# Optimization experiments

Measured on AMD Instinct MI355X. Metric: run time of the kernel, lower is better.

## Reference

```python
import jax, jax.numpy as jnp
import numpy as np

T, N, E = 8, 50000, 800000
XD, HD, GD, ZD, TD, YHD = 128, 256, 128, 128, 8, 16
PSH = 100          # ps_predictor hidden width
BN_EPS = 1e-5


def _dense(k, fan_in, shape):
    return jax.random.normal(k, shape, jnp.float32) * (1.0 / np.sqrt(fan_in))


def setup_inputs() -> dict:
    ks = jax.random.split(jax.random.key(0), 20)
    inp = {}
    inp["X"] = jax.random.normal(ks[0], (T, N, XD), jnp.float32)
    inp["C"] = jax.random.uniform(ks[1], (T, N, TD), dtype=jnp.float32)
    inp["Y_hist"] = jax.random.normal(ks[2], (T, N, YHD), jnp.float32)
    inp["edge_index"] = jax.random.randint(ks[3], (T, 2, E), 0, N)
    # parameters
    inp["phi_W"] = _dense(ks[4], XD, (XD, HD)); inp["phi_b"] = jnp.zeros((HD,), jnp.float32)
    inp["gc_W"] = _dense(ks[5], HD, (T, HD, GD)); inp["gc_b"] = jnp.zeros((T, GD), jnp.float32)
    inp["ew_logit"] = jax.random.normal(ks[6], (T, E), jnp.float32) * 0.1  # learned edge weights (pre-sigmoid)
    inp["fuse_W"] = _dense(ks[7], 2 * HD + GD, (2 * HD + GD, ZD)); inp["fuse_b"] = jnp.zeros((ZD,), jnp.float32)
    inp["o00_W"] = _dense(ks[8], ZD, (ZD, ZD)); inp["o00_b"] = jnp.zeros((ZD,), jnp.float32)
    inp["o10_W"] = _dense(ks[9], ZD, (ZD, ZD)); inp["o10_b"] = jnp.zeros((ZD,), jnp.float32)
    inp["o01_W"] = _dense(ks[10], ZD, (ZD, 1)); inp["o01_b"] = jnp.zeros((1,), jnp.float32)
    inp["o11_W"] = _dense(ks[11], ZD, (ZD, 1)); inp["o11_b"] = jnp.zeros((1,), jnp.float32)
    inp["ps1_W"] = _dense(ks[12], ZD, (ZD, PSH)); inp["ps1_b"] = jnp.zeros((PSH,), jnp.float32)
    inp["bn_g"] = jnp.ones((PSH,), jnp.float32); inp["bn_b"] = jnp.zeros((PSH,), jnp.float32)
    inp["ps2_W"] = _dense(ks[13], PSH, (PSH, 2)); inp["ps2_b"] = jnp.zeros((2,), jnp.float32)
    inp["gru_Wih"] = _dense(ks[14], ZD + TD + YHD, (3 * HD, ZD + TD + YHD))
    inp["gru_Whh"] = _dense(ks[15], HD, (3 * HD, HD))
    inp["gru_bih"] = jnp.zeros((3 * HD,), jnp.float32)
    inp["gru_bhh"] = jnp.zeros((3 * HD,), jnp.float32)
    return inp


def reference(X, C, Y_hist, edge_index, phi_W, phi_b, gc_W, gc_b, ew_logit,
              fuse_W, fuse_b, o00_W, o00_b, o10_W, o10_b, o01_W, o01_b,
              o11_W, o11_b, ps1_W, ps1_b, bn_g, bn_b, ps2_W, ps2_b,
              gru_Wih, gru_Whh, gru_bih, gru_bhh):
    h0 = jnp.zeros((N, HD), X.dtype)
    bn_scale = bn_g / jnp.sqrt(1.0 + BN_EPS)  # eval-mode BN: running_mean=0, running_var=1

    def step(h, xs):
        x, ei, c, yh, W_t, b_t, ewl_t = xs
        phi = jax.nn.relu(x @ phi_W + phi_b)                              # [N,HD]
        # --- GCNConv with learned sigmoid edge weights + self loops ---
        src, dst = ei[0], ei[1]
        ew = jax.nn.sigmoid(ewl_t)                                        # [E]
        deg = jax.ops.segment_sum(ew, dst, num_segments=N) + 1.0          # +1 for self-loop weight
        dinv = jax.lax.rsqrt(deg)
        norm = dinv[src] * ew * dinv[dst]                                 # symmetric norm per edge
        xw = phi @ W_t                                                    # [N,GD]
        agg = jax.ops.segment_sum(norm[:, None] * xw[src], dst, num_segments=N)
        agg = agg + xw / deg[:, None] + b_t                               # self-loop contribution + bias
        rep = jax.nn.relu(agg)                                            # [N,GD] (dropout off in eval)
        # --- fuse with skip connection ---
        z = jax.nn.relu(jnp.concatenate([h, rep, phi], axis=1) @ fuse_W + fuse_b)  # [N,ZD]
        # --- GRUCell (torch gate order: reset, update, new) ---
        inp = jnp.concatenate([z, c, yh], axis=1)
        gi = inp @ gru_Wih.T + gru_bih
        gh = h @ gru_Whh.T + gru_bhh
        i_r, i_z, i_n = jnp.split(gi, 3, axis=1)
        h_r, h_z, h_n = jnp.split(gh, 3, axis=1)
        r = jax.nn.sigmoid(i_r + h_r)
        u = jax.nn.sigmoid(i_z + h_z)
        n = jnp.tanh(i_n + r * h_n)
        h_new = (1.0 - u) * n + u * h
        # --- outcome heads ---
        y0 = jax.nn.relu(z @ o00_W + o00_b) @ o01_W + o01_b               # [N,1]
        y1 = jax.nn.relu(z @ o10_W + o10_b) @ o11_W + o11_b               # [N,1]
        # --- propensity head (BatchNorm eval, sigmoid, softmax) ---
        s = jax.nn.sigmoid((z @ ps1_W + ps1_b) * bn_scale + bn_b)
        ps = jax.nn.softmax(s @ ps2_W + ps2_b, axis=1)                    # [N,2]
        return h_new, (y1, y0, z, ps)

    h_fin, (all_y1, all_y0, all_z, all_ps) = jax.lax.scan(
        step, h0, (X, edge_index, C, Y_hist, gc_W, gc_b, ew_logit))
    return all_y1, all_y0, all_z, all_ps, h_fin
```

## Files before the change

### kernel.cpp

```cpp
#include <hip/hip_runtime.h>
#include <math.h>

#define T_STEPS 8
#define NN 50000
#define EE 800000
#define TN (T_STEPS*NN)
#define TE (T_STEPS*EE)

typedef unsigned int uint;
typedef unsigned short ushort;
typedef unsigned long long u64;
typedef __attribute__((ext_vector_type(8))) short short8;
typedef __attribute__((ext_vector_type(4))) float f32x4;

__device__ __forceinline__ float sigf(float x){ return 1.0f/(1.0f+expf(-x)); }
__device__ __forceinline__ ushort f2b(float f){
  uint x = __float_as_uint(f);
  uint r = (x + 0x7fffu + ((x>>16)&1u)) >> 16;
  return (ushort)r;
}
__device__ __forceinline__ float b2f(ushort u){ return __uint_as_float(((uint)u)<<16); }

__device__ __forceinline__ void gload16(const ushort* g, ushort* l){
  __builtin_amdgcn_global_load_lds(
      (const __attribute__((address_space(1))) void*)g,
      (__attribute__((address_space(3))) void*)l, 16, 0, 0);
}

template<int ROWS>
__device__ __forceinline__ void stage_tile(const ushort* base, int ld, int rowclamp,
                                           ushort* lds, int lane, int wid){
  constexpr int ITERS = ROWS/32;
#pragma unroll
  for (int i=0;i<ITERS;i++){
    int lin = i*256 + wid*64 + lane;
    int row = lin>>3, s = lin&7;
    int gr = row; if (gr > rowclamp) gr = rowclamp;
    const ushort* gp = base + (size_t)gr*ld + ((s ^ (row&7))<<3);
    gload16(gp, lds + (size_t)(i*256 + wid*64)*8);
  }
}

template<int ROWS>
__device__ __forceinline__ void stage512(const ushort* base, int ld, int rowclamp,
                                         ushort* lds, int tid){
  constexpr int ITERS = ROWS/64;
#pragma unroll
  for (int i=0;i<ITERS;i++){
    int lin = i*512 + tid;
    int row = lin>>3, s = lin&7;
    int gr = row; if (gr > rowclamp) gr = rowclamp;
    const ushort* gp = base + (size_t)gr*ld + ((s ^ (row&7))<<3);
    gload16(gp, lds + (size_t)lin*8);
  }
}

__device__ __forceinline__ short8 fragld(const ushort* lds, int R, int kk, int lane){
  int slot = (kk*4 + (lane>>4)) ^ (R&7);
  return *(const short8*)&lds[R*64 + slot*8];
}

struct Seg { const ushort* p; int ld; long ts; int w; };

__global__ __launch_bounds__(256,2) void gemm_bf(
    Seg s0, Seg s1, Seg s2,
    const ushort* __restrict__ W, int K2, long Wts,
    const float* __restrict__ bias, int act,
    const ushort* __restrict__ addp, int ldad, long adts,
    float* __restrict__ C32, int ldc, long c32ts,
    ushort* __restrict__ C16, int ldb, long c16ts,
    int Nrow, int NOvalid)
{
  __shared__ __align__(16) ushort As[8192];
  __shared__ __align__(16) ushort Bs[8192];
  const int t    = blockIdx.z;
  const int tid  = threadIdx.x;
  const int lane = tid & 63;
  const int wid  = __builtin_amdgcn_readfirstlane(tid >> 6);
  const int brow = blockIdx.x*128;
  const int bcol = blockIdx.y*128;
  const int wr = wid>>1, wc = wid&1;

  f32x4 acc[4][4];
#pragma unroll
  for(int m=0;m<4;m++)
#pragma unroll
    for(int n=0;n<4;n++) acc[m][n] = (f32x4){0.f,0.f,0.f,0.f};

  const int nk = K2 >> 6;
  for (int kt=0; kt<nk; ++kt){
    int col0 = kt*64;
    const ushort* ab; int ald;
    if (col0 < s0.w){ ab = s0.p + (size_t)t*s0.ts + col0; ald = s0.ld; }
    else if (col0 < s0.w + s1.w){ ab = s1.p + (size_t)t*s1.ts + (col0 - s0.w); ald = s1.ld; }
    else { ab = s2.p + (size_t)t*s2.ts + (col0 - s0.w - s1.w); ald = s2.ld; }
    stage_tile<128>(ab + (size_t)brow*ald, ald, Nrow-1-brow, As, lane, wid);
    stage_tile<128>(W + (size_t)t*Wts + (size_t)bcol*K2 + col0, K2, 1<<30, Bs, lane, wid);
    __syncthreads();
#pragma unroll
    for (int kk=0;kk<2;kk++){
      short8 a[4], b[4];
#pragma unroll
      for (int m=0;m<4;m++) a[m] = fragld(As, wr*64 + m*16 + (lane&15), kk, lane);
#pragma unroll
      for (int n=0;n<4;n++) b[n] = fragld(Bs, wc*64 + n*16 + (lane&15), kk, lane);
#pragma unroll
      for (int m=0;m<4;m++)
#pragma unroll
        for (int n=0;n<4;n++)
          acc[m][n] = __builtin_amdgcn_mfma_f32_16x16x32_bf16(a[m], b[n], acc[m][n], 0,0,0);
    }
    __syncthreads();
  }
  const int rbase = brow + wr*64 + (lane>>4)*4;
  const int cbase = bcol + wc*64 + (lane&15);
#pragma unroll
  for (int m=0;m<4;m++){
#pragma unroll
    for (int q=0;q<4;q++){
      int r = rbase + m*16 + q;
      if (r >= Nrow) continue;
#pragma unroll
      for (int n=0;n<4;n++){
        int c = cbase + n*16;
        if (c >= NOvalid) continue;
        float v = acc[m][n][q];
        if (addp) v += b2f(addp[(size_t)t*adts + (size_t)r*ldad + c]);
        if (bias) v += bias[c];
        if (act==1) v = fmaxf(v, 0.f);
        if (C32) C32[(size_t)t*c32ts + (size_t)r*ldc + c] = v;
        if (C16) C16[(size_t)t*c16ts + (size_t)r*ldb + c] = f2b(v);
      }
    }
  }
}

__global__ __launch_bounds__(512,2) void gemm_phi512(
    const float* __restrict__ A32,
    const ushort* __restrict__ W,
    const float* __restrict__ bias,
    ushort* __restrict__ C16, long c16ts,
    int Nrow)
{
  __shared__ __align__(16) ushort As[8192];
  __shared__ __align__(16) ushort Bs[16384];
  const int t    = blockIdx.z;
  const int tid  = threadIdx.x;
  const int lane = tid & 63;
  const int wid  = __builtin_amdgcn_readfirstlane(tid >> 6);
  const int brow = blockIdx.x*128;
  const int wr = wid>>2, wc = wid&3;
  const float* At = A32 + (size_t)t*NN*128;

  f32x4 acc[4][4];
#pragma unroll
  for(int m=0;m<4;m++)
#pragma unroll
    for(int n=0;n<4;n++) acc[m][n] = (f32x4){0.f,0.f,0.f,0.f};

  for (int kt=0; kt<2; ++kt){
    int col0 = kt*64;
#pragma unroll
    for (int it=0; it<4; ++it){
      int lin = it*512 + tid;
      int row = lin>>4, q4 = lin&15;
      int grow = brow + row; if (grow >= Nrow) grow = Nrow-1;
      float4 v = *(const float4*)&At[(size_t)grow*128 + col0 + q4*4];
      int s = q4>>1, half = q4&1;
      uint lo = (uint)f2b(v.x) | ((uint)f2b(v.y)<<16);
      uint hi = (uint)f2b(v.z) | ((uint)f2b(v.w)<<16);
      *(uint2*)&As[row*64 + ((s ^ (row&7))<<3) + half*4] = make_uint2(lo,hi);
    }
    stage512<256>(W + col0, 128, 1<<30, Bs, tid);
    __syncthreads();
#pragma unroll
    for (int kk=0;kk<2;kk++){
      short8 a[4], b[4];
#pragma unroll
      for (int m=0;m<4;m++) a[m] = fragld(As, wr*64 + m*16 + (lane&15), kk, lane);
#pragma unroll
      for (int n=0;n<4;n++) b[n] = fragld(Bs, wc*64 + n*16 + (lane&15), kk, lane);
#pragma unroll
      for (int m=0;m<4;m++)
#pragma unroll
        for (int n=0;n<4;n++)
          acc[m][n] = __builtin_amdgcn_mfma_f32_16x16x32_bf16(a[m], b[n], acc[m][n], 0,0,0);
    }
    __syncthreads();
  }
  const int rbase = brow + wr*64 + (lane>>4)*4;
  const int cbase = wc*64 + (lane&15);
#pragma unroll
  for (int m=0;m<4;m++){
#pragma unroll
    for (int q=0;q<4;q++){
      int r = rbase + m*16 + q;
      if (r >= Nrow) continue;
#pragma unroll
      for (int n=0;n<4;n++){
        int c = cbase + n*16;
        float v = acc[m][n][q] + bias[c];
        v = fmaxf(v, 0.f);
        C16[(size_t)t*c16ts + (size_t)r*256 + c] = f2b(v);
      }
    }
  }
}

__global__ __launch_bounds__(512,2) void gemm_gru512(
    Seg s0, Seg s1, Seg s2,
    const ushort* __restrict__ W,
    const float* __restrict__ bg,
    const float* __restrict__ hin,
    float* __restrict__ hout, ushort* __restrict__ hbfo,
    int Nrow)
{
  __shared__ __align__(16) ushort As[8192];
  __shared__ __align__(16) ushort Bs[16384];
  const int tid  = threadIdx.x;
  const int lane = tid & 63;
  const int wid  = __builtin_amdgcn_readfirstlane(tid >> 6);
  const int brow = blockIdx.x*128;
  const int bcol = blockIdx.y*256;
  const int wr = wid>>2, wc = wid&3;
  const int K2 = 448;

  f32x4 acc[4][4];
#pragma unroll
  for(int m=0;m<4;m++)
#pragma unroll
    for(int n=0;n<4;n++) acc[m][n] = (f32x4){0.f,0.f,0.f,0.f};

  for (int kt=0; kt<7; ++kt){
    int col0 = kt*64;
    const ushort* ab; int ald;
    if (col0 < s0.w){ ab = s0.p + col0; ald = s0.ld; }
    else if (col0 < s0.w + s1.w){ ab = s1.p + (col0 - s0.w); ald = s1.ld; }
    else { ab = s2.p + (col0 - s0.w - s1.w); ald = s2.ld; }
    stage512<128>(ab + (size_t)brow*ald, ald, Nrow-1-brow, As, tid);
    stage512<256>(W + (size_t)bcol*K2 + col0, K2, 1<<30, Bs, tid);
    __syncthreads();
#pragma unroll
    for (int kk=0;kk<2;kk++){
      short8 a[4], b[4];
#pragma unroll
      for (int m=0;m<4;m++) a[m] = fragld(As, wr*64 + m*16 + (lane&15), kk, lane);
#pragma unroll
      for (int n=0;n<4;n++) b[n] = fragld(Bs, wc*64 + n*16 + (lane&15), kk, lane);
#pragma unroll
      for (int m=0;m<4;m++)
#pragma unroll
        for (int n=0;n<4;n++)
          acc[m][n] = __builtin_amdgcn_mfma_f32_16x16x32_bf16(a[m], b[n], acc[m][n], 0,0,0);
    }
    __syncthreads();
  }
  const int jj = lane&15;
  const int G  = blockIdx.y*4 + wc;
  const int j  = G*16 + jj;
  const int rbase = brow + wr*64 + (lane>>4)*4;
  float bb[4];
#pragma unroll
  for (int n=0;n<4;n++) bb[n] = bg[G*64 + n*16 + jj];
#pragma unroll
  for (int m=0;m<4;m++){
#pragma unroll
    for (int q=0;q<4;q++){
      int r = rbase + m*16 + q;
      if (r >= Nrow) continue;
      float v0 = acc[m][0][q] + bb[0];
      float v1 = acc[m][1][q] + bb[1];
      float v2 = acc[m][2][q] + bb[2];
      float v3 = acc[m][3][q] + bb[3];
      float rg = sigf(v0), ug = sigf(v1);
      float ng = tanhf(v2 + rg*v3);
      float ho = hin[(size_t)r*256 + j];
      float hn = (1.f-ug)*ng + ug*ho;
      hout[(size_t)r*256 + j] = hn;
      hbfo[(size_t)r*256 + j] = f2b(hn);
    }
  }
}

__global__ __launch_bounds__(256,2) void heads_k(
    const ushort* __restrict__ Az, long Ats,
    const ushort* __restrict__ W,
    const float* __restrict__ o00b, const float* __restrict__ o10b,
    const float* __restrict__ w01, const float* __restrict__ b01,
    const float* __restrict__ w11, const float* __restrict__ b11,
    float* __restrict__ y0out, long y0ts,
    float* __restrict__ y1out, long y1ts, int Nrow)
{
  __shared__ __align__(16) ushort As[4096];
  __shared__ __align__(16) ushort Bs[16384];
  __shared__ float shy[4][64];
  const int t    = blockIdx.z;
  const int tid  = threadIdx.x;
  const int lane = tid & 63;
  const int wid  = __builtin_amdgcn_readfirstlane(tid >> 6);
  const int brow = blockIdx.x*64;
  const ushort* A = Az + (size_t)t*Ats;

  f32x4 acc[4][4];
#pragma unroll
  for(int m=0;m<4;m++)
#pragma unroll
    for(int n=0;n<4;n++) acc[m][n] = (f32x4){0.f,0.f,0.f,0.f};

  for (int kt=0; kt<2; ++kt){
    stage_tile<64>(A + (size_t)brow*128 + kt*64, 128, Nrow-1-brow, As, lane, wid);
    stage_tile<256>(W + kt*64, 128, 1<<30, Bs, lane, wid);
    __syncthreads();
#pragma unroll
    for (int kk=0;kk<2;kk++){
      short8 a[4], b[4];
#pragma unroll
      for (int m=0;m<4;m++) a[m] = fragld(As, m*16 + (lane&15), kk, lane);
#pragma unroll
      for (int n=0;n<4;n++) b[n] = fragld(Bs, wid*64 + n*16 + (lane&15), kk, lane);
#pragma unroll
      for (int m=0;m<4;m++)
#pragma unroll
        for (int n=0;n<4;n++)
          acc[m][n] = __builtin_amdgcn_mfma_f32_16x16x32_bf16(a[m], b[n], acc[m][n], 0,0,0);
    }
    __syncthreads();
  }
  float bb[4], ww[4];
#pragma unroll
  for (int n=0;n<4;n++){
    int c = wid*64 + n*16 + (lane&15);
    bb[n] = (c<128)? o00b[c] : o10b[c-128];
    ww[n] = (c<128)? w01[c]  : w11[c-128];
  }
#pragma unroll
  for (int m=0;m<4;m++){
#pragma unroll
    for (int q=0;q<4;q++){
      float p = 0.f;
#pragma unroll
      for (int n=0;n<4;n++) p += fmaxf(acc[m][n][q] + bb[n], 0.f) * ww[n];
#pragma unroll
      for (int o=1;o<16;o<<=1) p += __shfl_xor(p, o);
      if ((lane&15)==0) shy[wid][m*16 + (lane>>4)*4 + q] = p;
    }
  }
  __syncthreads();
  if (tid < 64){
    int r = brow + tid;
    if (r < Nrow){
      y0out[(size_t)t*y0ts + r] = shy[0][tid] + shy[1][tid] + b01[0];
      y1out[(size_t)t*y1ts + r] = shy[2][tid] + shy[3][tid] + b11[0];
    }
  }
}

__global__ __launch_bounds__(256,2) void ps_k(
    const ushort* __restrict__ Az, long Ats,
    const ushort* __restrict__ W,
    const float* __restrict__ psc, const float* __restrict__ psb,
    const float* __restrict__ W2, const float* __restrict__ b2,
    float* __restrict__ psout, long psts, int Nrow)
{
  __shared__ __align__(16) ushort As[8192];
  __shared__ __align__(16) ushort Bs[8192];
  __shared__ float sh0[2][128];
  __shared__ float sh1[2][128];
  const int t    = blockIdx.z;
  const int tid  = threadIdx.x;
  const int lane = tid & 63;
  const int wid  = __builtin_amdgcn_readfirstlane(tid >> 6);
  const int brow = blockIdx.x*128;
  const int wr = wid>>1, wc = wid&1;
  const ushort* A = Az + (size_t)t*Ats;

  f32x4 acc[4][4];
#pragma unroll
  for(int m=0;m<4;m++)
#pragma unroll
    for(int n=0;n<4;n++) acc[m][n] = (f32x4){0.f,0.f,0.f,0.f};

  for (int kt=0; kt<2; ++kt){
    stage_tile<128>(A + (size_t)brow*128 + kt*64, 128, Nrow-1-brow, As, lane, wid);
    stage_tile<128>(W + kt*64, 128, 1<<30, Bs, lane, wid);
    __syncthreads();
#pragma unroll
    for (int kk=0;kk<2;kk++){
      short8 a[4], b[4];
#pragma unroll
      for (int m=0;m<4;m++) a[m] = fragld(As, wr*64 + m*16 + (lane&15), kk, lane);
#pragma unroll
      for (int n=0;n<4;n++) b[n] = fragld(Bs, wc*64 + n*16 + (lane&15), kk, lane);
#pragma unroll
      for (int m=0;m<4;m++)
#pragma unroll
        for (int n=0;n<4;n++)
          acc[m][n] = __builtin_amdgcn_mfma_f32_16x16x32_bf16(a[m], b[n], acc[m][n], 0,0,0);
    }
    __syncthreads();
  }
  float sc[4], sb[4], w0_[4], w1_[4];
#pragma unroll
  for (int n=0;n<4;n++){
    int c = wc*64 + n*16 + (lane&15);
    bool ok = (c<100);
    sc[n] = ok? psc[c] : 0.f;
    sb[n] = ok? psb[c] : 0.f;
    w0_[n]= ok? W2[2*c] : 0.f;
    w1_[n]= ok? W2[2*c+1] : 0.f;
  }
#pragma unroll
  for (int m=0;m<4;m++){
#pragma unroll
    for (int q=0;q<4;q++){
      float a0=0.f, a1=0.f;
#pragma unroll
      for (int n=0;n<4;n++){
        float s = sigf(acc[m][n][q]*sc[n] + sb[n]);
        a0 += s*w0_[n]; a1 += s*w1_[n];
      }
#pragma unroll
      for (int o=1;o<16;o<<=1){ a0 += __shfl_xor(a0,o); a1 += __shfl_xor(a1,o); }
      if ((lane&15)==0){
        int rt = wr*64 + m*16 + (lane>>4)*4 + q;
        sh0[wc][rt] = a0; sh1[wc][rt] = a1;
      }
    }
  }
  __syncthreads();
  if (tid < 128){
    int r = brow + tid;
    if (r < Nrow){
      float l0 = sh0[0][tid]+sh0[1][tid]+b2[0];
      float l1 = sh1[0][tid]+sh1[1][tid]+b2[1];
      float mx = fmaxf(l0,l1);
      float e0 = expf(l0-mx), e1 = expf(l1-mx);
      float inv = 1.f/(e0+e1);
      psout[(size_t)t*psts + (size_t)r*2]   = e0*inv;
      psout[(size_t)t*psts + (size_t)r*2+1] = e1*inv;
    }
  }
}

__global__ void count_k(const int* __restrict__ ei, const float* __restrict__ ewl,
                        uint* __restrict__ degcnt, ushort* __restrict__ rank)
{
  int idx = blockIdx.x*256 + threadIdx.x;
  if (idx >= TE) return;
  int t = idx / EE;
  int e = idx - t*EE;
  const int* dst = ei + (size_t)t*2*EE + EE;
  int d = dst[e];
  uint v = (1u<<24) | (uint)(sigf(ewl[idx]) * 262144.0f);
  uint old = atomicAdd(&degcnt[t*NN + d], v);
  rank[idx] = (ushort)(old>>24);
}

__global__ void dinv_k(const uint* __restrict__ degcnt, int* __restrict__ cnt,
                       float* __restrict__ dnv, float* __restrict__ invd){
  int idx = blockIdx.x*256+threadIdx.x;
  if (idx>=TN) return;
  uint tot = degcnt[idx];
  int c = (int)(tot>>24);
  float S = (float)(tot & 0xFFFFFFu) * (1.f/262144.f);
  float dv = S + 1.f;
  cnt[idx] = c;
  dnv[idx]  = rsqrtf(dv);
  invd[idx] = 1.f/dv;
}

__global__ void scan1_k(const int* __restrict__ in, int* __restrict__ outv,
                        int* __restrict__ partials, int n)
{
  __shared__ int sh[256];
  int base = blockIdx.x*1024;
  int tid = threadIdx.x;
  int v[4]; int s=0;
#pragma unroll
  for (int i=0;i<4;i++){ int idx=base+tid*4+i; v[i] = (idx<n)? in[idx]:0; s+=v[i]; }
  sh[tid]=s; __syncthreads();
  for (int o=1;o<256;o<<=1){
    int t2 = (tid>=o)? sh[tid-o]:0;
    __syncthreads();
    sh[tid]+=t2;
    __syncthreads();
  }
  int excl = sh[tid]-s;
#pragma unroll
  for (int i=0;i<4;i++){ int idx=base+tid*4+i; if(idx<n) outv[idx]=excl; excl+=v[i]; }
  if (tid==255) partials[blockIdx.x]=sh[255];
}

__global__ void scan2_k(int* p, int np){
  __shared__ int sh[256];
  __shared__ int run;
  int tid=threadIdx.x;
  if(tid==0) run=0;
  __syncthreads();
  for(int base=0;base<np;base+=256){
    int v = (base+tid<np)? p[base+tid]:0;
    sh[tid]=v; __syncthreads();
    for(int o=1;o<256;o<<=1){
      int t2 = (tid>=o)? sh[tid-o]:0;
      __syncthreads();
      sh[tid]+=t2;
      __syncthreads();
    }
    int incl=sh[tid];
    int r0=run;
    __syncthreads();
    if(base+tid<np) p[base+tid]=r0+incl-v;
    __syncthreads();
    if(tid==0) run = r0 + sh[255];
    __syncthreads();
  }
}

__global__ void scan3_k(int* __restrict__ offs, const int* __restrict__ parts, int n){
  int idx = blockIdx.x*256+threadIdx.x;
  if (idx==0) offs[n] = TE;
  if (idx<n){ offs[idx] = offs[idx] + parts[idx>>10]; }
}

__global__ void fill_k(const int* __restrict__ ei, const float* __restrict__ ewl,
                       const float* __restrict__ dnv, const int* __restrict__ offs,
                       const ushort* __restrict__ rank, uint* __restrict__ epack)
{
  int idx = blockIdx.x*256 + threadIdx.x;
  if (idx >= TE) return;
  int t = idx / EE;
  int e = idx - t*EE;
  const int* srcp = ei + (size_t)t*2*EE;
  const int* dstp = srcp + EE;
  int s=srcp[e], d=dstp[e];
  float nr = dnv[t*NN+s] * sigf(ewl[idx]) * dnv[t*NN+d];
  uint nq = (uint)(nr*65535.f + 0.5f);
  int pos = offs[t*NN+d] + rank[idx];
  epack[pos] = (uint)s | (nq<<16);
}

__global__ __launch_bounds__(256) void gather_k(const int* __restrict__ offs,
    const uint* __restrict__ epack,
    const ushort* __restrict__ xwb, const float* __restrict__ invd,
    const float* __restrict__ gcb, ushort* __restrict__ rep)
{
  int bid  = blockIdx.x;
  int t    = bid & 7;
  int node = (bid>>3)*4 + (threadIdx.x>>6);
  int lane = threadIdx.x & 63;
  int half = lane>>5, ll = lane&31;
  if (node >= NN) return;
  const int* offs_t = offs + (size_t)t*NN;
  const ushort* xw_t = xwb + (size_t)t*NN*128;
  int o0 = offs_t[node], o1 = offs_t[node+1];
  float a0=0.f, a1=0.f, a2=0.f, a3=0.f;

  int j = o0 + half;
  for (; j+6 < o1; j += 8){
    uint e0 = epack[j],   e1 = epack[j+2];
    uint e2 = epack[j+4], e3 = epack[j+6];
    uint2 v0 = ((const uint2*)(xw_t + (size_t)(e0&0xffff)*128))[ll];
    uint2 v1 = ((const uint2*)(xw_t + (size_t)(e1&0xffff)*128))[ll];
    uint2 v2 = ((const uint2*)(xw_t + (size_t)(e2&0xffff)*128))[ll];
    uint2 v3 = ((const uint2*)(xw_t + (size_t)(e3&0xffff)*128))[ll];
    float n0 = (float)(e0>>16), n1 = (float)(e1>>16);
    float n2 = (float)(e2>>16), n3 = (float)(e3>>16);
    a0 = fmaf(n0, b2f((ushort)(v0.x&0xffff)), a0);
    a1 = fmaf(n0, b2f((ushort)(v0.x>>16)),   a1);
    a2 = fmaf(n0, b2f((ushort)(v0.y&0xffff)), a2);
    a3 = fmaf(n0, b2f((ushort)(v0.y>>16)),   a3);
    a0 = fmaf(n1, b2f((ushort)(v1.x&0xffff)), a0);
    a1 = fmaf(n1, b2f((ushort)(v1.x>>16)),   a1);
    a2 = fmaf(n1, b2f((ushort)(v1.y&0xffff)), a2);
    a3 = fmaf(n1, b2f((ushort)(v1.y>>16)),   a3);
    a0 = fmaf(n2, b2f((ushort)(v2.x&0xffff)), a0);
    a1 = fmaf(n2, b2f((ushort)(v2.x>>16)),   a1);
    a2 = fmaf(n2, b2f((ushort)(v2.y&0xffff)), a2);
    a3 = fmaf(n2, b2f((ushort)(v2.y>>16)),   a3);
    a0 = fmaf(n3, b2f((ushort)(v3.x&0xffff)), a0);
    a1 = fmaf(n3, b2f((ushort)(v3.x>>16)),   a1);
    a2 = fmaf(n3, b2f((ushort)(v3.y&0xffff)), a2);
    a3 = fmaf(n3, b2f((ushort)(v3.y>>16)),   a3);
  }
  for (; j < o1; j += 2){
    uint e0 = epack[j];
    uint2 v0 = ((const uint2*)(xw_t + (size_t)(e0&0xffff)*128))[ll];
    float n0 = (float)(e0>>16);
    a0 = fmaf(n0, b2f((ushort)(v0.x&0xffff)), a0);
    a1 = fmaf(n0, b2f((ushort)(v0.x>>16)),   a1);
    a2 = fmaf(n0, b2f((ushort)(v0.y&0xffff)), a2);
    a3 = fmaf(n0, b2f((ushort)(v0.y>>16)),   a3);
  }
  a0 += __shfl_xor(a0, 32);
  a1 += __shfl_xor(a1, 32);
  a2 += __shfl_xor(a2, 32);
  a3 += __shfl_xor(a3, 32);
  const float qs = 1.f/65535.f;
  a0 *= qs; a1 *= qs; a2 *= qs; a3 *= qs;
  float sl = invd[(size_t)t*NN + node];
  uint2 us = ((const uint2*)(xw_t + (size_t)node*128))[ll];
  float4 gb = ((const float4*)(gcb + (size_t)t*128))[ll];
  a0 = fmaf(sl, b2f((ushort)(us.x&0xffff)), a0) + gb.x;
  a1 = fmaf(sl, b2f((ushort)(us.x>>16)),   a1) + gb.y;
  a2 = fmaf(sl, b2f((ushort)(us.y&0xffff)), a2) + gb.z;
  a3 = fmaf(sl, b2f((ushort)(us.y>>16)),   a3) + gb.w;
  a0 = fmaxf(a0,0.f); a1 = fmaxf(a1,0.f);
  a2 = fmaxf(a2,0.f); a3 = fmaxf(a3,0.f);
  if (half==0){
    uint pk0 = (uint)f2b(a0) | ((uint)f2b(a1)<<16);
    uint pk1 = (uint)f2b(a2) | ((uint)f2b(a3)<<16);
    ((uint2*)(rep + ((size_t)t*NN + node)*128))[ll] = make_uint2(pk0, pk1);
  }
}

__global__ void convT_k(ushort* __restrict__ dst, const float* __restrict__ src,
                        int O, int Osrc, int K, int Kp)
{
  int idx = blockIdx.x*256 + threadIdx.x;
  if (idx >= O*Kp) return;
  dst += (size_t)blockIdx.y * O * Kp;
  src += (size_t)blockIdx.y * K * Osrc;
  int o = idx / Kp, k = idx - o*Kp;
  float v = (k<K && o<Osrc) ? src[(size_t)k*Osrc + o] : 0.f;
  dst[idx] = f2b(v);
}

__global__ void woc_k(ushort* __restrict__ dst, const float* __restrict__ o00W,
                      const float* __restrict__ o10W)
{
  int idx = blockIdx.x*256 + threadIdx.x;
  if (idx >= 256*128) return;
  int o = idx >> 7, k = idx & 127;
  float v = (o<128) ? o00W[(size_t)k*128 + o] : o10W[(size_t)k*128 + (o-128)];
  dst[idx] = f2b(v);
}

__global__ void wgru_k(const float* __restrict__ Wih, const float* __restrict__ Whh,
                       const float* __restrict__ bih, const float* __restrict__ bhh,
                       ushort* __restrict__ Wg, float* __restrict__ bg)
{
  int idx = blockIdx.x*256 + threadIdx.x;
  if (idx >= 1024*448) return;
  int c = idx/448, k = idx - c*448;
  int G = c>>6, g = (c>>4)&3, jj = c&15;
  int j = G*16 + jj;
  float v = 0.f;
  if (k < 152){
    if      (g==0) v = Wih[(size_t)j*152 + k];
    else if (g==1) v = Wih[(size_t)(256+j)*152 + k];
    else if (g==2) v = Wih[(size_t)(512+j)*152 + k];
  } else if (k >= 192){
    int kk = k-192;
    if      (g==0) v = Whh[(size_t)j*256 + kk];
    else if (g==1) v = Whh[(size_t)(256+j)*256 + kk];
    else if (g==3) v = Whh[(size_t)(512+j)*256 + kk];
  }
  Wg[idx] = f2b(v);
  if (k==0){
    float b;
    if      (g==0) b = bih[j]     + bhh[j];
    else if (g==1) b = bih[256+j] + bhh[256+j];
    else if (g==2) b = bih[512+j];
    else           b = bhh[512+j];
    bg[c] = b;
  }
}

__global__ void misc_k(const float* __restrict__ ps1b, const float* __restrict__ bng,
                       const float* __restrict__ bnb,
                       float* __restrict__ psc, float* __restrict__ psb)
{
  int i = threadIdx.x;
  if (i<100){ float sc = bng[i]*rsqrtf(1.f+1e-5f); psc[i]=sc; psb[i]=ps1b[i]*sc+bnb[i]; }
  else if (i<128){ psc[i]=0.f; psb[i]=0.f; }
}

__global__ void cyh_k(ushort* __restrict__ cyh, const float* __restrict__ Cc,
                      const float* __restrict__ Yh)
{
  long gid = (long)blockIdx.x*256 + threadIdx.x;
  if (gid >= (long)TN*64) return;
  long g = gid >> 6; int l = (int)(gid & 63);
  float v = 0.f;
  if (l < 8)       v = Cc[g*8 + l];
  else if (l < 24) v = Yh[g*16 + (l-8)];
  cyh[g*64 + l] = f2b(v);
}

extern "C" void kernel_launch(void* const* d_in, const int* in_sizes, int n_in,
                              void* d_out_v, int out_size, void* d_ws, size_t ws_size,
                              hipStream_t stream)
{
  const float* X    = (const float*)d_in[0];
  const float* Cc   = (const float*)d_in[1];
  const float* Yh   = (const float*)d_in[2];
  const int*   EI   = (const int*)  d_in[3];
  const float* phiW = (const float*)d_in[4];  const float* phib = (const float*)d_in[5];
  const float* gcW  = (const float*)d_in[6];  const float* gcb  = (const float*)d_in[7];
  const float* ewl  = (const float*)d_in[8];
  const float* fuseW= (const float*)d_in[9];  const float* fuseb= (const float*)d_in[10];
  const float* o00W = (const float*)d_in[11]; const float* o00b = (const float*)d_in[12];
  const float* o10W = (const float*)d_in[13]; const float* o10b = (const float*)d_in[14];
  const float* o01W = (const float*)d_in[15]; const float* o01b = (const float*)d_in[16];
  const float* o11W = (const float*)d_in[17]; const float* o11b = (const float*)d_in[18];
  const float* ps1W = (const float*)d_in[19]; const float* ps1b = (const float*)d_in[20];
  const float* bng  = (const float*)d_in[21]; const float* bnb  = (const float*)d_in[22];
  const float* ps2W = (const float*)d_in[23]; const float* ps2b = (const float*)d_in[24];
  const float* Wih  = (const float*)d_in[25]; const float* Whh  = (const float*)d_in[26];
  const float* bih  = (const float*)d_in[27]; const float* bhh  = (const float*)d_in[28];
  float* out = (float*)d_out_v;

  char* wsb = (char*)d_ws;
  size_t off=0;
  auto alloc=[&](size_t bytes)->void*{
    void* p = wsb + off;
    off = (off + bytes + 255) & ~(size_t)255;
    return p;
  };
  uint*  degcnt= (uint*) alloc((size_t)TN*4);
  int*   cnt   = (int*)  alloc((size_t)TN*4);
  int*   offs  = (int*)  alloc(((size_t)TN+1)*4);
  float* dnv   = (float*)alloc((size_t)TN*4);
  float* invd  = (float*)alloc((size_t)TN*4);
  uint*  epack = (uint*) alloc((size_t)TE*4);
  ushort* rankb= (ushort*)alloc((size_t)TE*2);
  int*   parts = (int*)  alloc(4096);
  ushort* rep_all = (ushort*)alloc((size_t)TN*128*2);
  ushort* phiA = (ushort*)alloc((size_t)TN*256*2);
  ushort* xwb  = (ushort*)alloc((size_t)TN*128*2);
  ushort* pz   = (ushort*)alloc((size_t)TN*128*2);
  ushort* hbf0 = (ushort*)alloc((size_t)NN*256*2);
  ushort* hbf1 = (ushort*)alloc((size_t)NN*256*2);
  float*  hb   = (float*)alloc((size_t)NN*256*4);
  ushort* phiWt= (ushort*)alloc(256*128*2);
  ushort* gcWt = (ushort*)alloc((size_t)T_STEPS*128*256*2);
  ushort* WhT  = (ushort*)alloc(128*256*2);
  ushort* WrpT = (ushort*)alloc(128*384*2);
  ushort* Wgru = (ushort*)alloc((size_t)1024*448*2);
  float* bgru  = (float*)alloc(1024*4);
  ushort* wocT = (ushort*)alloc(256*128*2);
  ushort* ps1T = (ushort*)alloc(128*128*2);
  float* psc   = (float*)alloc(128*4);
  float* psb   = (float*)alloc(128*4);

  ushort* zbf     = phiA;
  ushort* cyh     = phiA + (size_t)TN*128;

  hipMemsetAsync(degcnt, 0, (size_t)TN*4, stream);
  hipMemsetAsync(hb,   0, (size_t)NN*256*4, stream);
  hipMemsetAsync(hbf0, 0, (size_t)NN*256*2, stream);

  misc_k<<<1,256,0,stream>>>(ps1b,bng,bnb,psc,psb);
  convT_k<<<dim3((256*128+255)/256,1),256,0,stream>>>(phiWt, phiW, 256,256,128,128);
  convT_k<<<dim3((128*256+255)/256,T_STEPS),256,0,stream>>>(gcWt, gcW, 128,128,256,256);
  convT_k<<<dim3((128*256+255)/256,1),256,0,stream>>>(WhT, fuseW, 128,128,256,256);
  convT_k<<<dim3((128*384+255)/256,1),256,0,stream>>>(WrpT, fuseW+256*128, 128,128,384,384);
  convT_k<<<dim3((128*128+255)/256,1),256,0,stream>>>(ps1T, ps1W, 128,100,128,128);
  wgru_k<<<(1024*448+255)/256,256,0,stream>>>(Wih,Whh,bih,bhh,Wgru,bgru);
  woc_k<<<(256*128+255)/256,256,0,stream>>>(wocT, o00W, o10W);

  count_k<<<(TE+255)/256,256,0,stream>>>(EI,ewl,degcnt,rankb);
  dinv_k<<<(TN+255)/256,256,0,stream>>>(degcnt,cnt,dnv,invd);
  scan1_k<<<(TN+1023)/1024,256,0,stream>>>(cnt,offs,parts,TN);
  scan2_k<<<1,256,0,stream>>>(parts,(TN+1023)/1024);
  scan3_k<<<(TN+255)/256,256,0,stream>>>(offs,parts,TN);
  fill_k<<<(TE+255)/256,256,0,stream>>>(EI,ewl,dnv,offs,rankb,epack);

  const size_t zoff  = (size_t)2*TN;
  const size_t psoff = zoff + (size_t)TN*128;
  const size_t hoff  = psoff + (size_t)TN*2;
  constexpr int GX = (NN+127)/128;
  const Seg S0 = {nullptr,0,0,0};

  gemm_phi512<<<dim3(GX,1,8),512,0,stream>>>(
    X, phiWt, phib, phiA, (long)NN*256, NN);
  gemm_bf<<<dim3(GX,1,8),256,0,stream>>>(
    Seg{phiA,256,(long)NN*256,256}, S0, S0, gcWt,256,(long)128*256, nullptr,0,
    nullptr,0,0, nullptr,0,0, xwb,128,(long)NN*128, NN,128);
  gather_k<<<(NN/4)*8,256,0,stream>>>(offs, epack, xwb, invd, gcb, rep_all);
  gemm_bf<<<dim3(GX,1,8),256,0,stream>>>(
    Seg{rep_all,128,(long)NN*128,128}, Seg{phiA,256,(long)NN*256,256}, S0,
    WrpT,384,0, nullptr,0,
    nullptr,0,0, nullptr,0,0, pz,128,(long)NN*128, NN,128);
  cyh_k<<<(int)(((long)TN*64+255)/256),256,0,stream>>>(cyh, Cc, Yh);

  for (int t=0;t<T_STEPS;t++){
    const ushort* hbi = (t&1)? hbf1 : hbf0;
    ushort*       hbo = (t&1)? hbf0 : hbf1;
    float* hout = (t==T_STEPS-1)? (out+hoff) : hb;
    float* zt = out + zoff + (size_t)t*NN*128;
    ushort* zbt = zbf + (size_t)t*NN*128;
    gemm_bf<<<dim3(GX,1,1),256,0,stream>>>(
      Seg{hbi,256,0,256}, S0, S0, WhT,256,0, fuseb,1,
      pz + (size_t)t*NN*128,128,0, zt,128,0, zbt,128,0, NN,128);
    gemm_gru512<<<dim3(GX,4),512,0,stream>>>(
      Seg{zbt,128,0,128}, Seg{cyh + (size_t)t*NN*64,64,0,64}, Seg{hbi,256,0,256},
      Wgru, bgru, hb, hout, hbo, NN);
  }

  heads_k<<<dim3((NN+63)/64,1,8),256,0,stream>>>(
    zbf,(long)NN*128, wocT, o00b,o10b, o01W,o01b, o11W,o11b,
    out + TN, (long)NN,
    out, (long)NN, NN);
  ps_k<<<dim3(GX,1,8),256,0,stream>>>(
    zbf,(long)NN*128, ps1T, psc,psb, ps2W,ps2b,
    out+psoff, (long)NN*2, NN);

  (void)in_sizes; (void)n_in; (void)out_size; (void)ws_size;
}
```

Measured before the change: 2.294 ms.

## Fuse edge counting with phi GEMM and edge fill with XW GEMM

Merges the edge degree-count kernel and the phi projection GEMM into one launch, with blocks split by index. It likewise merges the CSR fill kernel with the per-step graph-conv XW GEMM, so memory-bound atomic and scatter work can overlap with MFMA compute and two launches go away. A dedicated XW GEMM kernel with a fixed 128-column tile replaces the generic gemm_bf call. The cost is heavier blocks that share shared-memory allocation and launch bounds with the light edge blocks, which may lower occupancy for the edge work.

```diff
diff --git a/kernel.cpp b/kernel.cpp
--- a/kernel.cpp
+++ b/kernel.cpp
@@ -6,6 +6,9 @@
 #define EE 800000
 #define TN (T_STEPS*NN)
 #define TE (T_STEPS*EE)
+#define GX 391
+#define CPB 12500
+#define FPB 25000
 
 typedef unsigned int uint;
 typedef unsigned short ushort;
@@ -135,20 +138,34 @@
   }
 }
 
-__global__ __launch_bounds__(512,2) void gemm_phi512(
-    const float* __restrict__ A32,
-    const ushort* __restrict__ W,
+__global__ __launch_bounds__(512,2) void count_phi_k(
+    const int* __restrict__ ei, const float* __restrict__ ewl,
+    uint* __restrict__ degcnt, ushort* __restrict__ rank,
+    const float* __restrict__ A32, const ushort* __restrict__ W,
     const float* __restrict__ bias,
-    ushort* __restrict__ C16, long c16ts,
-    int Nrow)
+    ushort* __restrict__ C16, long c16ts, int Nrow)
 {
   __shared__ __align__(16) ushort As[8192];
   __shared__ __align__(16) ushort Bs[16384];
-  const int t    = blockIdx.z;
+  if (blockIdx.x < CPB){
+    int idx = blockIdx.x*512 + threadIdx.x;
+    if (idx >= TE) return;
+    int t = idx / EE;
+    int e = idx - t*EE;
+    const int* dst = ei + (size_t)t*2*EE + EE;
+    int d = dst[e];
+    uint v = (1u<<24) | (uint)(sigf(ewl[idx]) * 262144.0f);
+    uint old = atomicAdd(&degcnt[t*NN + d], v);
+    rank[idx] = (ushort)(old>>24);
+    return;
+  }
+  const int pb   = blockIdx.x - CPB;
+  const int t    = pb / GX;
+  const int bx   = pb - t*GX;
   const int tid  = threadIdx.x;
   const int lane = tid & 63;
   const int wid  = __builtin_amdgcn_readfirstlane(tid >> 6);
-  const int brow = blockIdx.x*128;
+  const int brow = bx*128;
   const int wr = wid>>2, wc = wid&3;
   const float* At = A32 + (size_t)t*NN*128;
 
@@ -202,6 +219,83 @@
         float v = acc[m][n][q] + bias[c];
         v = fmaxf(v, 0.f);
         C16[(size_t)t*c16ts + (size_t)r*256 + c] = f2b(v);
+      }
+    }
+  }
+}
+
+__global__ __launch_bounds__(256,2) void fill_xw_k(
+    const int* __restrict__ ei, const float* __restrict__ ewl,
+    const float* __restrict__ dnv, const int* __restrict__ offs,
+    const ushort* __restrict__ rank, uint* __restrict__ epack,
+    const ushort* __restrict__ phiA, const ushort* __restrict__ gcWt,
+    ushort* __restrict__ xwb, int Nrow)
+{
+  __shared__ __align__(16) ushort As[8192];
+  __shared__ __align__(16) ushort Bs[8192];
+  if (blockIdx.x < FPB){
+    int idx = blockIdx.x*256 + threadIdx.x;
+    if (idx >= TE) return;
+    int t = idx / EE;
+    int e = idx - t*EE;
+    const int* srcp = ei + (size_t)t*2*EE;
+    const int* dstp = srcp + EE;
+    int s=srcp[e], d=dstp[e];
+    float nr = dnv[t*NN+s] * sigf(ewl[idx]) * dnv[t*NN+d];
+    uint nq = (uint)(nr*65535.f + 0.5f);
+    int pos = offs[t*NN+d] + rank[idx];
+    epack[pos] = (uint)s | (nq<<16);
+    return;
+  }
+  const int pb   = blockIdx.x - FPB;
+  const int t    = pb / GX;
+  const int bx   = pb - t*GX;
+  const int tid  = threadIdx.x;
+  const int lane = tid & 63;
+  const int wid  = __builtin_amdgcn_readfirstlane(tid >> 6);
+  const int brow = bx*128;
+  const int wr = wid>>1, wc = wid&1;
+  const ushort* A = phiA + (size_t)t*NN*256;
+  const ushort* W = gcWt + (size_t)t*128*256;
+
+  f32x4 acc[4][4];
+#pragma unroll
+  for(int m=0;m<4;m++)
+#pragma unroll
+    for(int n=0;n<4;n++) acc[m][n] = (f32x4){0.f,0.f,0.f,0.f};
+
+  for (int kt=0; kt<4; ++kt){
+    int col0 = kt*64;
+    stage_tile<128>(A + (size_t)brow*256 + col0, 256, Nrow-1-brow, As, lane, wid);
+    stage_tile<128>(W + col0, 256, 1<<30, Bs, lane, wid);
+    __syncthreads();
+#pragma unroll
+    for (int kk=0;kk<2;kk++){
+      short8 a[4], b[4];
+#pragma unroll
+      for (int m=0;m<4;m++) a[m] = fragld(As, wr*64 + m*16 + (lane&15), kk, lane);
+#pragma unroll
+      for (int n=0;n<4;n++) b[n] = fragld(Bs, wc*64 + n*16 + (lane&15), kk, lane);
+#pragma unroll
+      for (int m=0;m<4;m++)
+#pragma unroll
+        for (int n=0;n<4;n++)
+          acc[m][n] = __builtin_amdgcn_mfma_f32_16x16x32_bf16(a[m], b[n], acc[m][n], 0,0,0);
+    }
+    __syncthreads();
+  }
+  const int rbase = brow + wr*64 + (lane>>4)*4;
+  const int cbase = wc*64 + (lane&15);
+#pragma unroll
+  for (int m=0;m<4;m++){
+#pragma unroll
+    for (int q=0;q<4;q++){
+      int r = rbase + m*16 + q;
+      if (r >= Nrow) continue;
+#pragma unroll
+      for (int n=0;n<4;n++){
+        int c = cbase + n*16;
+        xwb[(size_t)t*NN*128 + (size_t)r*128 + c] = f2b(acc[m][n][q]);
       }
     }
   }
@@ -440,20 +534,6 @@
       psout[(size_t)t*psts + (size_t)r*2+1] = e1*inv;
     }
   }
-}
-
-__global__ void count_k(const int* __restrict__ ei, const float* __restrict__ ewl,
-                        uint* __restrict__ degcnt, ushort* __restrict__ rank)
-{
-  int idx = blockIdx.x*256 + threadIdx.x;
-  if (idx >= TE) return;
-  int t = idx / EE;
-  int e = idx - t*EE;
-  const int* dst = ei + (size_t)t*2*EE + EE;
-  int d = dst[e];
-  uint v = (1u<<24) | (uint)(sigf(ewl[idx]) * 262144.0f);
-  uint old = atomicAdd(&degcnt[t*NN + d], v);
-  rank[idx] = (ushort)(old>>24);
 }
 
 __global__ void dinv_k(const uint* __restrict__ degcnt, int* __restrict__ cnt,
@@ -520,23 +600,6 @@
   int idx = blockIdx.x*256+threadIdx.x;
   if (idx==0) offs[n] = TE;
   if (idx<n){ offs[idx] = offs[idx] + parts[idx>>10]; }
-}
-
-__global__ void fill_k(const int* __restrict__ ei, const float* __restrict__ ewl,
-                       const float* __restrict__ dnv, const int* __restrict__ offs,
-                       const ushort* __restrict__ rank, uint* __restrict__ epack)
-{
-  int idx = blockIdx.x*256 + threadIdx.x;
-  if (idx >= TE) return;
-  int t = idx / EE;
-  int e = idx - t*EE;
-  const int* srcp = ei + (size_t)t*2*EE;
-  const int* dstp = srcp + EE;
-  int s=srcp[e], d=dstp[e];
-  float nr = dnv[t*NN+s] * sigf(ewl[idx]) * dnv[t*NN+d];
-  uint nq = (uint)(nr*65535.f + 0.5f);
-  int pos = offs[t*NN+d] + rank[idx];
-  epack[pos] = (uint)s | (nq<<16);
 }
 
 __global__ __launch_bounds__(256) void gather_k(const int* __restrict__ offs,
@@ -759,24 +822,20 @@
   wgru_k<<<(1024*448+255)/256,256,0,stream>>>(Wih,Whh,bih,bhh,Wgru,bgru);
   woc_k<<<(256*128+255)/256,256,0,stream>>>(wocT, o00W, o10W);
 
-  count_k<<<(TE+255)/256,256,0,stream>>>(EI,ewl,degcnt,rankb);
+  count_phi_k<<<CPB + GX*8, 512, 0, stream>>>(
+    EI, ewl, degcnt, rankb, X, phiWt, phib, phiA, (long)NN*256, NN);
   dinv_k<<<(TN+255)/256,256,0,stream>>>(degcnt,cnt,dnv,invd);
   scan1_k<<<(TN+1023)/1024,256,0,stream>>>(cnt,offs,parts,TN);
   scan2_k<<<1,256,0,stream>>>(parts,(TN+1023)/1024);
   scan3_k<<<(TN+255)/256,256,0,stream>>>(offs,parts,TN);
-  fill_k<<<(TE+255)/256,256,0,stream>>>(EI,ewl,dnv,offs,rankb,epack);
+  fill_xw_k<<<FPB + GX*8, 256, 0, stream>>>(
+    EI, ewl, dnv, offs, rankb, epack, phiA, gcWt, xwb, NN);
 
   const size_t zoff  = (size_t)2*TN;
   const size_t psoff = zoff + (size_t)TN*128;
   const size_t hoff  = psoff + (size_t)TN*2;
-  constexpr int GX = (NN+127)/128;
   const Seg S0 = {nullptr,0,0,0};
 
-  gemm_phi512<<<dim3(GX,1,8),512,0,stream>>>(
-    X, phiWt, phib, phiA, (long)NN*256, NN);
-  gemm_bf<<<dim3(GX,1,8),256,0,stream>>>(
-    Seg{phiA,256,(long)NN*256,256}, S0, S0, gcWt,256,(long)128*256, nullptr,0,
-    nullptr,0,0, nullptr,0,0, xwb,128,(long)NN*128, NN,128);
   gather_k<<<(NN/4)*8,256,0,stream>>>(offs, epack, xwb, invd, gcb, rep_all);
   gemm_bf<<<dim3(GX,1,8),256,0,stream>>>(
     Seg{rep_all,128,(long)NN*128,128}, Seg{phiA,256,(long)NN*256,256}, S0,
```

Measured after the change: 2.320 ms. No clear change (+1.1%).
